# Performance work log

Measured on AMD Instinct MI355X. Metric: run time of the kernel, lower is better.

## Reference

```python
import jax, jax.numpy as jnp
import numpy as np

B, P, D = 256, 256, 514          # batch, num_patches (16^2), model_dim
H, HD = 8, 64                    # n_heads, head_dim ((D-2)//H)
SH = 256                         # shared_hidden = head_mlp_hidden_dims[0]
HH = 256                         # per-head hidden (head_mlp_hidden_dims[1])
DFF = 2048                       # ffn hidden
LH = 2 * SH                      # lat_modulator hidden = shared_hidden*2
LD = D - 2                       # learnable_dim

def gelu(x):
    return jax.nn.gelu(x, approximate=False)  # torch nn.GELU default is exact erf

def setup_inputs() -> dict:
    key = jax.random.key(0)
    ks = jax.random.split(key, 16)
    s = 0.02
    x = jax.random.normal(ks[0], (B, P, D), dtype=jnp.float32)
    # shared spatial layer: Linear(P -> SH), torch weight layout [out, in]
    Ws = jax.random.normal(ks[1], (SH, P), dtype=jnp.float32) * s
    bs = jax.random.normal(ks[2], (SH,), dtype=jnp.float32) * s
    # lat modulator: Linear(2 -> LH), GELU, Linear(LH -> 2*SH) with special init
    LW1 = jax.random.normal(ks[3], (LH, 2), dtype=jnp.float32) * s
    Lb1 = jax.random.normal(ks[4], (LH,), dtype=jnp.float32) * s
    LW2 = jnp.zeros((2 * SH, LH), dtype=jnp.float32)  # zeroed per module init
    Lb2 = jnp.concatenate([jnp.ones((SH,), jnp.float32), jnp.zeros((SH,), jnp.float32)])
    # per-head processing: Linear(SH->HH), GELU, Linear(HH->P), stacked over heads
    HW1 = jax.random.normal(ks[5], (H, HH, SH), dtype=jnp.float32) * s
    Hb1 = jax.random.normal(ks[6], (H, HH), dtype=jnp.float32) * s
    HW2 = jax.random.normal(ks[7], (H, P, HH), dtype=jnp.float32) * s
    Hb2 = jax.random.normal(ks[8], (H, P), dtype=jnp.float32) * s
    # ffn: Linear(D -> DFF) with last-2 input cols zeroed, GELU, Linear(DFF -> LD)
    FW1 = jax.random.normal(ks[9], (DFF, D), dtype=jnp.float32) * s
    FW1 = FW1.at[:, -2:].set(0.0)
    Fb1 = jax.random.normal(ks[10], (DFF,), dtype=jnp.float32) * s
    FW2 = jax.random.normal(ks[11], (LD, DFF), dtype=jnp.float32) * s
    Fb2 = jax.random.normal(ks[12], (LD,), dtype=jnp.float32) * s
    return dict(x=x, Ws=Ws, bs=bs, LW1=LW1, Lb1=Lb1, LW2=LW2, Lb2=Lb2,
                HW1=HW1, Hb1=Hb1, HW2=HW2, Hb2=Hb2,
                FW1=FW1, Fb1=Fb1, FW2=FW2, Fb2=Fb2)

def reference(x, Ws, bs, LW1, Lb1, LW2, Lb2, HW1, Hb1, HW2, Hb2, FW1, Fb1, FW2, Fb2):
    central = P // 2
    sc_central = x[:, central, -2:]          # [B, 2]
    sc_all = x[:, :, -2:]                    # [B, P, 2]
    x_learn = x[:, :, :-2]                   # [B, P, LD]
    x_res = x_learn
    # all heads at once: [B, P, H, HD] -> [B, H, HD, P]
    xh = x_learn.reshape(B, P, H, HD).transpose(0, 2, 3, 1)
    shared = jnp.einsum('bhdp,op->bhdo', xh, Ws) + bs   # [B, H, HD, SH]
    # FiLM params (loop-invariant in original, hoisted here)
    mod = gelu(sc_central @ LW1.T + Lb1) @ LW2.T + Lb2  # [B, 2*SH]
    gamma = mod[:, :SH][:, None, None, :]
    beta = mod[:, SH:][:, None, None, :]
    shared = shared * gamma + beta
    # per-head MLPs as grouped GEMMs
    h = gelu(jnp.einsum('bhdo,hko->bhdk', shared, HW1) + Hb1[None, :, None, :])
    out = jnp.einsum('bhdk,hpk->bhdp', h, HW2) + Hb2[None, :, None, :]  # [B,H,HD,P]
    x_learn = out.transpose(0, 3, 1, 2).reshape(B, P, LD) + x_res
    x_full = jnp.concatenate([x_learn, sc_all], axis=-1)  # [B, P, D]
    f = gelu(x_full @ FW1.T + Fb1) @ FW2.T + Fb2          # [B, P, LD]
    x_learn = f + x_learn
    return jnp.concatenate([x_learn, sc_all], axis=-1)
```

## Files before the change

kernel.cpp:

```cpp
#include <hip/hip_runtime.h>
#include <math.h>

typedef __attribute__((ext_vector_type(8))) __bf16 bf16x8;
typedef __attribute__((ext_vector_type(4))) float f32x4;
typedef __attribute__((ext_vector_type(2))) float f32x2;

#define DEV __device__ __forceinline__

typedef __attribute__((address_space(3))) unsigned int lds_u32;
typedef __attribute__((address_space(1))) unsigned int glb_u32;

DEV unsigned short f2bf(float f) {
    unsigned int u = __builtin_bit_cast(unsigned int, f);
    u += 0x7FFFu + ((u >> 16) & 1u);
    return (unsigned short)(u >> 16);
}
DEV float bf2f(unsigned short u) {
    unsigned int v = (unsigned int)u << 16;
    return __builtin_bit_cast(float, v);
}
DEV unsigned int pack2(float a, float b) {
    return (unsigned int)f2bf(a) | ((unsigned int)f2bf(b) << 16);
}
DEV float gelu_exact(float v) {
    return 0.5f * v * (1.0f + erff(v * 0.70710678118654752f));
}
DEV float gelu_fast(float x) {
    float z = 1.5957691216f * x + 0.0713548163f * x * x * x;
    float e = __expf(-z);
    return x * __builtin_amdgcn_rcpf(1.0f + e);
}

__global__ void cast_bf16_kernel(const float* __restrict__ src,
                                 unsigned short* __restrict__ dst, int n) {
    int i = blockIdx.x * 256 + threadIdx.x;
    if (i < n) dst[i] = f2bf(src[i]);
}

__global__ void cast_fw1_kernel(const float* __restrict__ src,
                                unsigned short* __restrict__ dst) {
    int i = blockIdx.x * 256 + threadIdx.x;
    if (i < 2048 * 512) {
        int row = i >> 9, k = i & 511;
        dst[i] = f2bf(src[row * 514 + k]);
    }
}

__global__ void gb_kernel(const float* __restrict__ x,
                          const float* __restrict__ LW1, const float* __restrict__ Lb1,
                          const float* __restrict__ LW2, const float* __restrict__ Lb2,
                          float* __restrict__ gb) {
    __shared__ float t[8][512];
    const int b0 = blockIdx.x * 8, tid = threadIdx.x;
    for (int idx = tid; idx < 8 * 512; idx += 256) {
        int bb = idx >> 9, j = idx & 511;
        float s0 = x[((size_t)(b0 + bb) * 256 + 128) * 514 + 512];
        float s1 = x[((size_t)(b0 + bb) * 256 + 128) * 514 + 513];
        t[bb][j] = gelu_exact(LW1[j * 2] * s0 + LW1[j * 2 + 1] * s1 + Lb1[j]);
    }
    __syncthreads();
    const int i = tid;
    float a0[8], a1[8];
    float l0 = Lb2[i], l1 = Lb2[i + 256];
    #pragma unroll
    for (int bb = 0; bb < 8; ++bb) { a0[bb] = l0; a1[bb] = l1; }
    for (int j = 0; j < 512; ++j) {
        float w0 = LW2[(size_t)i * 512 + j];
        float w1 = LW2[(size_t)(i + 256) * 512 + j];
        #pragma unroll
        for (int bb = 0; bb < 8; ++bb) {
            a0[bb] += w0 * t[bb][j];
            a1[bb] += w1 * t[bb][j];
        }
    }
    #pragma unroll
    for (int bb = 0; bb < 8; ++bb) {
        gb[(size_t)(b0 + bb) * 512 + i] = a0[bb];
        gb[(size_t)(b0 + bb) * 512 + i + 256] = a1[bb];
    }
}

__global__ void sc_copy_kernel(const float* __restrict__ x, float* __restrict__ out,
                               float* __restrict__ scbuf) {
    size_t idx = (size_t)blockIdx.x * 256 + threadIdx.x;
    size_t off = idx * 514 + 512;
    f32x2 v = *(const f32x2*)(x + off);
    *(f32x2*)(out + off) = v;
    *(f32x2*)(scbuf + idx * 2) = v;
}

#define MPAD 264

__global__ __launch_bounds__(256, 2) void mixer_kernel(
    const float* __restrict__ x, const float* __restrict__ bs,
    const float* __restrict__ Hb1, const float* __restrict__ Hb2,
    const unsigned short* __restrict__ Wsb,
    const unsigned short* __restrict__ HW1b,
    const unsigned short* __restrict__ HW2b,
    const float* __restrict__ gb,
    unsigned short* __restrict__ Xb) {
    __shared__ __attribute__((aligned(16))) char smem[33792 + 34816];
    unsigned short* XT = (unsigned short*)smem;
    unsigned short* S = (unsigned short*)(smem + 33792);
    unsigned short* ST = S;

    const int bid = blockIdx.x;
    const int b = bid >> 3;
    const int h = bid & 7;
    const int tid = threadIdx.x;
    const int lane = tid & 63;
    const int w = tid >> 6;
    const int l15 = lane & 15;
    const int l4 = lane >> 4;

    {
        const int c = lane;
        const float* xp = x + ((size_t)b * 256) * 514 + (size_t)h * 64 + c;
        for (int i = 0; i < 32; ++i) {
            int p = (i * 4 + w) * 2;
            float v0 = xp[(size_t)p * 514];
            float v1 = xp[(size_t)(p + 1) * 514];
            *(unsigned int*)&XT[c * MPAD + p] = pack2(v0, v1);
        }
    }
    __syncthreads();

    f32x4 acc[4][4];

    #pragma unroll
    for (int mt = 0; mt < 4; ++mt)
        #pragma unroll
        for (int nt = 0; nt < 4; ++nt) acc[mt][nt] = 0.f;
    {
        bf16x8 bnx[4];
        #pragma unroll
        for (int nt = 0; nt < 4; ++nt)
            bnx[nt] = *(const bf16x8*)(Wsb + (size_t)(w * 64 + nt * 16 + l15) * 256 + l4 * 8);
        for (int kc = 0; kc < 8; ++kc) {
            bf16x8 bcur[4];
            #pragma unroll
            for (int nt = 0; nt < 4; ++nt) bcur[nt] = bnx[nt];
            if (kc < 7) {
                #pragma unroll
                for (int nt = 0; nt < 4; ++nt)
                    bnx[nt] = *(const bf16x8*)(Wsb + (size_t)(w * 64 + nt * 16 + l15) * 256 + (kc + 1) * 32 + l4 * 8);
            }
            #pragma unroll
            for (int mt = 0; mt < 4; ++mt) {
                bf16x8 afr = *(const bf16x8*)&XT[(mt * 16 + l15) * MPAD + kc * 32 + l4 * 8];
                #pragma unroll
                for (int nt = 0; nt < 4; ++nt)
                    acc[mt][nt] = __builtin_amdgcn_mfma_f32_16x16x32_bf16(afr, bcur[nt], acc[mt][nt], 0, 0, 0);
            }
        }
    }
    #pragma unroll
    for (int nt = 0; nt < 4; ++nt) {
        int o = w * 64 + nt * 16 + l15;
        float bsv = bs[o];
        float g = gb[(size_t)b * 512 + o];
        float be = gb[(size_t)b * 512 + 256 + o];
        #pragma unroll
        for (int mt = 0; mt < 4; ++mt)
            #pragma unroll
            for (int r = 0; r < 4; ++r) {
                int c = mt * 16 + l4 * 4 + r;
                S[c * MPAD + o] = f2bf((acc[mt][nt][r] + bsv) * g + be);
            }
    }
    __syncthreads();

    const unsigned short* W2p = HW1b + (size_t)h * 65536;
    #pragma unroll
    for (int mt = 0; mt < 4; ++mt)
        #pragma unroll
        for (int nt = 0; nt < 4; ++nt) acc[mt][nt] = 0.f;
    {
        bf16x8 bnx[4];
        #pragma unroll
        for (int nt = 0; nt < 4; ++nt)
            bnx[nt] = *(const bf16x8*)(W2p + (size_t)(w * 64 + nt * 16 + l15) * 256 + l4 * 8);
        for (int kc = 0; kc < 8; ++kc) {
            bf16x8 bcur[4];
            #pragma unroll
            for (int nt = 0; nt < 4; ++nt) bcur[nt] = bnx[nt];
            if (kc < 7) {
                #pragma unroll
                for (int nt = 0; nt < 4; ++nt)
                    bnx[nt] = *(const bf16x8*)(W2p + (size_t)(w * 64 + nt * 16 + l15) * 256 + (kc + 1) * 32 + l4 * 8);
            }
            #pragma unroll
            for (int mt = 0; mt < 4; ++mt) {
                bf16x8 afr = *(const bf16x8*)&S[(mt * 16 + l15) * MPAD + kc * 32 + l4 * 8];
                #pragma unroll
                for (int nt = 0; nt < 4; ++nt)
                    acc[mt][nt] = __builtin_amdgcn_mfma_f32_16x16x32_bf16(afr, bcur[nt], acc[mt][nt], 0, 0, 0);
            }
        }
    }
    __syncthreads();
    #pragma unroll
    for (int nt = 0; nt < 4; ++nt) {
        int kk = w * 64 + nt * 16 + l15;
        float hb = Hb1[(size_t)h * 256 + kk];
        #pragma unroll
        for (int mt = 0; mt < 4; ++mt)
            #pragma unroll
            for (int r = 0; r < 4; ++r) {
                int c = mt * 16 + l4 * 4 + r;
                S[c * MPAD + kk] = f2bf(gelu_fast(acc[mt][nt][r] + hb));
            }
    }
    __syncthreads();

    const unsigned short* W3p = HW2b + (size_t)h * 65536;
    #pragma unroll
    for (int mt = 0; mt < 4; ++mt)
        #pragma unroll
        for (int nt = 0; nt < 4; ++nt) acc[mt][nt] = 0.f;
    {
        bf16x8 bnx[4];
        #pragma unroll
        for (int nt = 0; nt < 4; ++nt)
            bnx[nt] = *(const bf16x8*)(W3p + (size_t)(w * 64 + nt * 16 + l15) * 256 + l4 * 8);
        for (int kc = 0; kc < 8; ++kc) {
            bf16x8 bcur[4];
            #pragma unroll
            for (int nt = 0; nt < 4; ++nt) bcur[nt] = bnx[nt];
            if (kc < 7) {
                #pragma unroll
                for (int nt = 0; nt < 4; ++nt)
                    bnx[nt] = *(const bf16x8*)(W3p + (size_t)(w * 64 + nt * 16 + l15) * 256 + (kc + 1) * 32 + l4 * 8);
            }
            #pragma unroll
            for (int mt = 0; mt < 4; ++mt) {
                bf16x8 afr = *(const bf16x8*)&S[(mt * 16 + l15) * MPAD + kc * 32 + l4 * 8];
                #pragma unroll
                for (int nt = 0; nt < 4; ++nt)
                    acc[mt][nt] = __builtin_amdgcn_mfma_f32_16x16x32_bf16(afr, bcur[nt], acc[mt][nt], 0, 0, 0);
            }
        }
    }
    __syncthreads();

    #pragma unroll
    for (int nt = 0; nt < 4; ++nt) {
        int p = w * 64 + nt * 16 + l15;
        float hb = Hb2[(size_t)h * 256 + p];
        #pragma unroll
        for (int mt = 0; mt < 4; ++mt) {
            int c0 = mt * 16 + l4 * 4;
            ushort4 uv;
            uv.x = f2bf(acc[mt][nt][0] + hb + bf2f(XT[(c0 + 0) * MPAD + p]));
            uv.y = f2bf(acc[mt][nt][1] + hb + bf2f(XT[(c0 + 1) * MPAD + p]));
            uv.z = f2bf(acc[mt][nt][2] + hb + bf2f(XT[(c0 + 2) * MPAD + p]));
            uv.w = f2bf(acc[mt][nt][3] + hb + bf2f(XT[(c0 + 3) * MPAD + p]));
            *(ushort4*)(ST + p * 68 + c0) = uv;
        }
    }
    __syncthreads();

    #pragma unroll
    for (int s = 0; s < 16; ++s) {
        int row = s * 16 + w * 4 + l4;
        ushort4 u = *(const ushort4*)(ST + row * 68 + l15 * 4);
        *(ushort4*)(Xb + ((size_t)(b * 256 + row)) * 512 + h * 64 + l15 * 4) = u;
    }
}

DEV void stage_half(const unsigned short* g, size_t gstride, int row0, int k0,
                    char* half_base, int w, int lane) {
    const int slot = lane & 7;
    const int r8 = lane >> 3;
    const int swz = (slot ^ r8) * 16;
    #pragma unroll
    for (int i = 0; i < 2; ++i) {
        int chunk = w * 2 + i;
        int row = chunk * 8 + r8;
        const char* src = (const char*)(g + (size_t)(row0 + row) * gstride + k0) + swz;
        __builtin_amdgcn_global_load_lds((const glb_u32*)src,
                                         (lds_u32*)(half_base + chunk * 1024), 16, 0, 0);
    }
}

DEV void stage4(const unsigned short* A, size_t sA, int m0,
                const unsigned short* B, size_t sB, int n0, int k0,
                char* Abuf, char* Bbuf, int w, int lane) {
    stage_half(A, sA, m0, k0, Abuf, w, lane);
    stage_half(A, sA, m0 + 128, k0, Abuf + 16384, w, lane);
    stage_half(B, sB, n0, k0, Bbuf, w, lane);
    stage_half(B, sB, n0 + 128, k0, Bbuf + 16384, w, lane);
}

DEV void tile_body(const unsigned short* A, size_t sA, int m0,
                   const unsigned short* B, size_t sB, int n0,
                   char* smem, int cb, int kn, bool more,
                   int vA0, int vA1, int vB0, int vB1,
                   int w, int lane, f32x4 (&acc)[8][4]) {
    if (more) {
        int nb = 32768 - cb;
        stage4(A, sA, m0, B, sB, n0, kn, smem + nb, smem + 65536 + nb, w, lane);
    }
    __builtin_amdgcn_s_setprio(1);
    #pragma unroll
    for (int kk = 0; kk < 2; ++kk) {
        const int vA = kk ? vA1 : vA0;
        const int vB = kk ? vB1 : vB0;
        bf16x8 bf[4];
        #pragma unroll
        for (int nf = 0; nf < 4; ++nf)
            bf[nf] = *(const bf16x8*)(smem + vB + cb + nf * 2048);
        #pragma unroll
        for (int mh = 0; mh < 2; ++mh) {
            bf16x8 af[4];
            #pragma unroll
            for (int mf = 0; mf < 4; ++mf)
                af[mf] = *(const bf16x8*)(smem + vA + cb + mh * 8192 + mf * 2048);
            #pragma unroll
            for (int mf = 0; mf < 4; ++mf)
                #pragma unroll
                for (int nf = 0; nf < 4; ++nf)
                    acc[mh * 4 + mf][nf] = __builtin_amdgcn_mfma_f32_16x16x32_bf16(
                        af[mf], bf[nf], acc[mh * 4 + mf][nf], 0, 0, 0);
        }
    }
    __builtin_amdgcn_s_setprio(0);
    if (more) asm volatile("s_waitcnt vmcnt(0)" ::: "memory");
    __builtin_amdgcn_s_barrier();
}

DEV void gemm_loop(const unsigned short* A, size_t sA,
                   const unsigned short* B, size_t sB,
                   int m0, int n0, int NT,
                   char* smem, int w, int lane, f32x4 (&acc)[8][4]) {
    const int wm = w >> 2, wn = w & 3;
    const int l15 = lane & 15, l4 = lane >> 4;
    const int sw = (l15 & 7) << 4;
    const int k0off = (l4 * 16) ^ sw;
    const int k1off = (64 + l4 * 16) ^ sw;
    const int aBase = (wm * 128 + l15) * 128;
    const int bBase = 65536 + (wn * 64 + l15) * 128;
    const int vA0 = aBase + k0off, vA1 = aBase + k1off;
    const int vB0 = bBase + k0off, vB1 = bBase + k1off;

    stage4(A, sA, m0, B, sB, n0, 0, smem, smem + 65536, w, lane);
    asm volatile("s_waitcnt vmcnt(0)" ::: "memory");
    __builtin_amdgcn_s_barrier();

    for (int t = 0; t < NT; t += 2) {
        tile_body(A, sA, m0, B, sB, n0, smem, 0, (t + 1) * 64, t + 1 < NT,
                  vA0, vA1, vB0, vB1, w, lane, acc);
        tile_body(A, sA, m0, B, sB, n0, smem, 32768, (t + 2) * 64, t + 2 < NT,
                  vA0, vA1, vB0, vB1, w, lane, acc);
    }
}

__global__ __launch_bounds__(512, 1) void gemm1_kernel(
    const unsigned short* __restrict__ A,
    const unsigned short* __restrict__ B,
    const float* __restrict__ Fb1,
    const float* __restrict__ FW1,
    const float* __restrict__ scbuf,
    long pass_m0,
    unsigned short* __restrict__ G) {
    __shared__ __attribute__((aligned(16))) char smem[131072];

    const int nwg = gridDim.x;
    const int cpx = nwg >> 3;
    const int bid = (blockIdx.x & 7) * cpx + (blockIdx.x >> 3);
    const int m0 = (bid >> 3) * 256;
    const int n0 = (bid & 7) * 256;
    const int tid = threadIdx.x;
    const int lane = tid & 63;
    const int w = tid >> 6;
    const int l15 = lane & 15;
    const int l4 = lane >> 4;
    const int wm = w >> 2, wn = w & 3;

    f32x4 acc[8][4];
    #pragma unroll
    for (int mf = 0; mf < 8; ++mf)
        #pragma unroll
        for (int nf = 0; nf < 4; ++nf) acc[mf][nf] = 0.f;

    gemm_loop(A, 512, B, 512, m0, n0, 8, smem, w, lane, acc);

    float fb[4], wa[4], wb[4];
    #pragma unroll
    for (int nf = 0; nf < 4; ++nf) {
        int n = n0 + wn * 64 + nf * 16 + l15;
        fb[nf] = Fb1[n];
        wa[nf] = FW1[(size_t)n * 514 + 512];
        wb[nf] = FW1[(size_t)n * 514 + 513];
    }
    unsigned short* LT = (unsigned short*)smem;
    #pragma unroll
    for (int ph = 0; ph < 2; ++ph) {
        if (wm == ph) {
            #pragma unroll
            for (int mfg = 0; mfg < 8; ++mfg) {
                f32x2 sc[4];
                #pragma unroll
                for (int r = 0; r < 4; ++r) {
                    long rowg = pass_m0 + m0 + ph * 128 + mfg * 16 + l4 * 4 + r;
                    sc[r] = *(const f32x2*)(scbuf + rowg * 2);
                }
                #pragma unroll
                for (int nf = 0; nf < 4; ++nf)
                    #pragma unroll
                    for (int r = 0; r < 4; ++r) {
                        float v = acc[mfg][nf][r] + fb[nf] + sc[r].x * wa[nf] + sc[r].y * wb[nf];
                        int rl = mfg * 16 + l4 * 4 + r;
                        LT[rl * 264 + wn * 64 + nf * 16 + l15] = f2bf(gelu_fast(v));
                    }
            }
        }
        __syncthreads();
        {
            const int row16 = tid >> 5, col16 = tid & 31;
            #pragma unroll
            for (int sp = 0; sp < 8; ++sp) {
                int row = sp * 16 + row16;
                uint4 d = *(const uint4*)((const char*)smem + row * 528 + col16 * 16);
                *(uint4*)(G + ((size_t)(m0 + ph * 128 + row)) * 2048 + n0 + col16 * 8) = d;
            }
        }
        __syncthreads();
    }
}

__global__ __launch_bounds__(512, 1) void gemm2_kernel(
    const unsigned short* __restrict__ A,
    const unsigned short* __restrict__ B,
    const float* __restrict__ Fb2,
    const unsigned short* __restrict__ Xb,
    long pass_m0,
    float* __restrict__ io) {
    __shared__ __attribute__((aligned(16))) char smem[131072];

    const int nwg = gridDim.x;
    const int cpx = nwg >> 3;
    const int bid = (blockIdx.x & 7) * cpx + (blockIdx.x >> 3);
    const int m0 = (bid >> 1) * 256;
    const int n0 = (bid & 1) * 256;
    const int tid = threadIdx.x;
    const int lane = tid & 63;
    const int w = tid >> 6;
    const int l15 = lane & 15;
    const int l4 = lane >> 4;
    const int wm = w >> 2, wn = w & 3;

    f32x4 acc[8][4];
    #pragma unroll
    for (int mf = 0; mf < 8; ++mf)
        #pragma unroll
        for (int nf = 0; nf < 4; ++nf) acc[mf][nf] = 0.f;

    gemm_loop(A, 2048, B, 2048, m0, n0, 32, smem, w, lane, acc);

    #pragma unroll
    for (int nf = 0; nf < 4; ++nf) {
        int n = n0 + wn * 64 + nf * 16 + l15;
        float fbv = Fb2[n];
        #pragma unroll
        for (int mfg = 0; mfg < 8; ++mfg)
            #pragma unroll
            for (int r = 0; r < 4; ++r) {
                long rowg = pass_m0 + m0 + wm * 128 + mfg * 16 + l4 * 4 + r;
                float resv = bf2f(Xb[(size_t)rowg * 512 + n]);
                io[rowg * 514 + n] = acc[mfg][nf][r] + fbv + resv;
            }
    }
}

extern "C" void kernel_launch(void* const* d_in, const int* in_sizes, int n_in,
                              void* d_out, int out_size, void* d_ws, size_t ws_size,
                              hipStream_t stream) {
    const float* x = (const float*)d_in[0];
    const float* Ws = (const float*)d_in[1];
    const float* bs = (const float*)d_in[2];
    const float* LW1 = (const float*)d_in[3];
    const float* Lb1 = (const float*)d_in[4];
    const float* LW2 = (const float*)d_in[5];
    const float* Lb2 = (const float*)d_in[6];
    const float* HW1 = (const float*)d_in[7];
    const float* Hb1 = (const float*)d_in[8];
    const float* HW2 = (const float*)d_in[9];
    const float* Hb2 = (const float*)d_in[10];
    const float* FW1 = (const float*)d_in[11];
    const float* Fb1 = (const float*)d_in[12];
    const float* FW2 = (const float*)d_in[13];
    const float* Fb2 = (const float*)d_in[14];
    float* out = (float*)d_out;

    char* ws = (char*)d_ws;
    unsigned short* Wsb = (unsigned short*)(ws);
    unsigned short* HW1b = (unsigned short*)(ws + 131072);
    unsigned short* HW2b = (unsigned short*)(ws + 1179648);
    unsigned short* FW1b = (unsigned short*)(ws + 2228224);
    unsigned short* FW2b = (unsigned short*)(ws + 4325376);
    float* gb = (float*)(ws + 6422528);
    float* scbuf = (float*)(ws + 6946816);
    unsigned short* Xb = (unsigned short*)(ws + 7471104);
    unsigned short* Gbuf = (unsigned short*)(ws + 7471104 + 67108864);

    const size_t fixed = 7471104 + 67108864;
    int npass = 32;
    for (int np = 2; np <= 32; np *= 2) {
        if (fixed + (size_t)268435456 / np <= ws_size) { npass = np; break; }
    }
    const long Mtot = 65536;
    const long Mp = Mtot / npass;

    cast_bf16_kernel<<<256, 256, 0, stream>>>(Ws, Wsb, 65536);
    cast_bf16_kernel<<<2048, 256, 0, stream>>>(HW1, HW1b, 524288);
    cast_bf16_kernel<<<2048, 256, 0, stream>>>(HW2, HW2b, 524288);
    cast_bf16_kernel<<<4096, 256, 0, stream>>>(FW2, FW2b, 1048576);
    cast_fw1_kernel<<<4096, 256, 0, stream>>>(FW1, FW1b);
    gb_kernel<<<32, 256, 0, stream>>>(x, LW1, Lb1, LW2, Lb2, gb);
    sc_copy_kernel<<<256, 256, 0, stream>>>(x, out, scbuf);

    mixer_kernel<<<2048, 256, 0, stream>>>(x, bs, Hb1, Hb2, Wsb, HW1b, HW2b, gb, Xb);

    for (int p = 0; p < npass; ++p) {
        long m0 = (long)p * Mp;
        gemm1_kernel<<<(int)(Mp / 256) * 8, 512, 0, stream>>>(
            Xb + m0 * 512, FW1b, Fb1, FW1, scbuf, m0, Gbuf);
        gemm2_kernel<<<(int)(Mp / 256) * 2, 512, 0, stream>>>(
            Gbuf, FW2b, Fb2, Xb, m0, out);
    }
}
```

Baseline: 665.8 us.

## Shrink GEMM tiles to 128x128 with 256 threads and several blocks per CU

The FFN GEMM kernels drop the 256x256, 512-thread, single-block-per-CU double-buffered pipeline and use 128x128 tiles with 4 waves and a simple single-buffer stage/sync loop. Each block uses about 33KB of LDS, so three blocks can share a CU and overlap load latency through occupancy instead of explicit prefetch. The epilogues shrink to match, and the mixer's transposing load now reads 8 consecutive patches per thread and writes them with one 16-byte LDS store. In exchange the smaller tiles lower operand reuse, adding global and LDS traffic per FLOP, and the explicit software pipelining is lost.

```diff
diff --git a/kernel.cpp b/kernel.cpp
--- a/kernel.cpp
+++ b/kernel.cpp
@@ -116,11 +116,23 @@
     {
         const int c = lane;
         const float* xp = x + ((size_t)b * 256) * 514 + (size_t)h * 64 + c;
-        for (int i = 0; i < 32; ++i) {
-            int p = (i * 4 + w) * 2;
-            float v0 = xp[(size_t)p * 514];
-            float v1 = xp[(size_t)(p + 1) * 514];
-            *(unsigned int*)&XT[c * MPAD + p] = pack2(v0, v1);
+        #pragma unroll
+        for (int g = 0; g < 8; ++g) {
+            int p0 = w * 64 + g * 8;
+            float v0 = xp[(size_t)(p0 + 0) * 514];
+            float v1 = xp[(size_t)(p0 + 1) * 514];
+            float v2 = xp[(size_t)(p0 + 2) * 514];
+            float v3 = xp[(size_t)(p0 + 3) * 514];
+            float v4 = xp[(size_t)(p0 + 4) * 514];
+            float v5 = xp[(size_t)(p0 + 5) * 514];
+            float v6 = xp[(size_t)(p0 + 6) * 514];
+            float v7 = xp[(size_t)(p0 + 7) * 514];
+            uint4 pk;
+            pk.x = pack2(v0, v1);
+            pk.y = pack2(v2, v3);
+            pk.z = pack2(v4, v5);
+            pk.w = pack2(v6, v7);
+            *(uint4*)&XT[c * MPAD + p0] = pk;
         }
     }
     __syncthreads();
@@ -268,94 +280,60 @@
     }
 }
 
-DEV void stage_half(const unsigned short* g, size_t gstride, int row0, int k0,
-                    char* half_base, int w, int lane) {
-    const int slot = lane & 7;
-    const int r8 = lane >> 3;
+DEV void stage_m97(const unsigned short* g, size_t gstride, int row0, int k0,
+                   char* lbuf, int tid) {
+    const int slot = tid & 7;
+    const int r8 = (tid >> 3) & 7;
+    const int wv = tid >> 6;
     const int swz = (slot ^ r8) * 16;
     #pragma unroll
-    for (int i = 0; i < 2; ++i) {
-        int chunk = w * 2 + i;
+    for (int i = 0; i < 4; ++i) {
+        int chunk = i * 4 + wv;
         int row = chunk * 8 + r8;
         const char* src = (const char*)(g + (size_t)(row0 + row) * gstride + k0) + swz;
         __builtin_amdgcn_global_load_lds((const glb_u32*)src,
-                                         (lds_u32*)(half_base + chunk * 1024), 16, 0, 0);
-    }
-}
-
-DEV void stage4(const unsigned short* A, size_t sA, int m0,
-                const unsigned short* B, size_t sB, int n0, int k0,
-                char* Abuf, char* Bbuf, int w, int lane) {
-    stage_half(A, sA, m0, k0, Abuf, w, lane);
-    stage_half(A, sA, m0 + 128, k0, Abuf + 16384, w, lane);
-    stage_half(B, sB, n0, k0, Bbuf, w, lane);
-    stage_half(B, sB, n0 + 128, k0, Bbuf + 16384, w, lane);
-}
-
-DEV void tile_body(const unsigned short* A, size_t sA, int m0,
-                   const unsigned short* B, size_t sB, int n0,
-                   char* smem, int cb, int kn, bool more,
-                   int vA0, int vA1, int vB0, int vB1,
-                   int w, int lane, f32x4 (&acc)[8][4]) {
-    if (more) {
-        int nb = 32768 - cb;
-        stage4(A, sA, m0, B, sB, n0, kn, smem + nb, smem + 65536 + nb, w, lane);
-    }
-    __builtin_amdgcn_s_setprio(1);
-    #pragma unroll
-    for (int kk = 0; kk < 2; ++kk) {
-        const int vA = kk ? vA1 : vA0;
-        const int vB = kk ? vB1 : vB0;
-        bf16x8 bf[4];
-        #pragma unroll
-        for (int nf = 0; nf < 4; ++nf)
-            bf[nf] = *(const bf16x8*)(smem + vB + cb + nf * 2048);
-        #pragma unroll
-        for (int mh = 0; mh < 2; ++mh) {
-            bf16x8 af[4];
+                                         (lds_u32*)(lbuf + chunk * 1024), 16, 0, 0);
+    }
+}
+
+DEV void gemm_loop97(const unsigned short* A, size_t sA,
+                     const unsigned short* B, size_t sB,
+                     int m0, int n0, int NT,
+                     char* smem, int tid, f32x4 (&acc)[4][4]) {
+    const int lane = tid & 63;
+    const int w = tid >> 6;
+    const int l15 = lane & 15, l4 = lane >> 4;
+    const int wm = w >> 1, wn = w & 1;
+
+    for (int t = 0; t < NT; ++t) {
+        stage_m97(A, sA, m0, t * 64, smem, tid);
+        stage_m97(B, sB, n0, t * 64, smem + 16384, tid);
+        __syncthreads();
+        #pragma unroll
+        for (int kk = 0; kk < 2; ++kk) {
+            bf16x8 af[4], bf[4];
+            #pragma unroll
+            for (int mf = 0; mf < 4; ++mf) {
+                int row = wm * 64 + mf * 16 + l15;
+                af[mf] = *(const bf16x8*)(smem + row * 128 + ((kk * 64 + l4 * 16) ^ ((row & 7) << 4)));
+            }
+            #pragma unroll
+            for (int nf = 0; nf < 4; ++nf) {
+                int row = wn * 64 + nf * 16 + l15;
+                bf[nf] = *(const bf16x8*)(smem + 16384 + row * 128 + ((kk * 64 + l4 * 16) ^ ((row & 7) << 4)));
+            }
             #pragma unroll
             for (int mf = 0; mf < 4; ++mf)
-                af[mf] = *(const bf16x8*)(smem + vA + cb + mh * 8192 + mf * 2048);
-            #pragma unroll
-            for (int mf = 0; mf < 4; ++mf)
                 #pragma unroll
                 for (int nf = 0; nf < 4; ++nf)
-                    acc[mh * 4 + mf][nf] = __builtin_amdgcn_mfma_f32_16x16x32_bf16(
-                        af[mf], bf[nf], acc[mh * 4 + mf][nf], 0, 0, 0);
-        }
-    }
-    __builtin_amdgcn_s_setprio(0);
-    if (more) asm volatile("s_waitcnt vmcnt(0)" ::: "memory");
-    __builtin_amdgcn_s_barrier();
-}
-
-DEV void gemm_loop(const unsigned short* A, size_t sA,
-                   const unsigned short* B, size_t sB,
-                   int m0, int n0, int NT,
-                   char* smem, int w, int lane, f32x4 (&acc)[8][4]) {
-    const int wm = w >> 2, wn = w & 3;
-    const int l15 = lane & 15, l4 = lane >> 4;
-    const int sw = (l15 & 7) << 4;
-    const int k0off = (l4 * 16) ^ sw;
-    const int k1off = (64 + l4 * 16) ^ sw;
-    const int aBase = (wm * 128 + l15) * 128;
-    const int bBase = 65536 + (wn * 64 + l15) * 128;
-    const int vA0 = aBase + k0off, vA1 = aBase + k1off;
-    const int vB0 = bBase + k0off, vB1 = bBase + k1off;
-
-    stage4(A, sA, m0, B, sB, n0, 0, smem, smem + 65536, w, lane);
-    asm volatile("s_waitcnt vmcnt(0)" ::: "memory");
-    __builtin_amdgcn_s_barrier();
-
-    for (int t = 0; t < NT; t += 2) {
-        tile_body(A, sA, m0, B, sB, n0, smem, 0, (t + 1) * 64, t + 1 < NT,
-                  vA0, vA1, vB0, vB1, w, lane, acc);
-        tile_body(A, sA, m0, B, sB, n0, smem, 32768, (t + 2) * 64, t + 2 < NT,
-                  vA0, vA1, vB0, vB1, w, lane, acc);
-    }
-}
-
-__global__ __launch_bounds__(512, 1) void gemm1_kernel(
+                    acc[mf][nf] = __builtin_amdgcn_mfma_f32_16x16x32_bf16(
+                        af[mf], bf[nf], acc[mf][nf], 0, 0, 0);
+        }
+        __syncthreads();
+    }
+}
+
+__global__ __launch_bounds__(256, 3) void gemm1_kernel(
     const unsigned short* __restrict__ A,
     const unsigned short* __restrict__ B,
     const float* __restrict__ Fb1,
@@ -363,27 +341,27 @@
     const float* __restrict__ scbuf,
     long pass_m0,
     unsigned short* __restrict__ G) {
-    __shared__ __attribute__((aligned(16))) char smem[131072];
+    __shared__ __attribute__((aligned(16))) char smem[34816];
 
     const int nwg = gridDim.x;
     const int cpx = nwg >> 3;
     const int bid = (blockIdx.x & 7) * cpx + (blockIdx.x >> 3);
-    const int m0 = (bid >> 3) * 256;
-    const int n0 = (bid & 7) * 256;
+    const int m0 = (bid >> 4) * 128;
+    const int n0 = (bid & 15) * 128;
     const int tid = threadIdx.x;
     const int lane = tid & 63;
     const int w = tid >> 6;
     const int l15 = lane & 15;
     const int l4 = lane >> 4;
-    const int wm = w >> 2, wn = w & 3;
-
-    f32x4 acc[8][4];
-    #pragma unroll
-    for (int mf = 0; mf < 8; ++mf)
+    const int wm = w >> 1, wn = w & 1;
+
+    f32x4 acc[4][4];
+    #pragma unroll
+    for (int mf = 0; mf < 4; ++mf)
         #pragma unroll
         for (int nf = 0; nf < 4; ++nf) acc[mf][nf] = 0.f;
 
-    gemm_loop(A, 512, B, 512, m0, n0, 8, smem, w, lane, acc);
+    gemm_loop97(A, 512, B, 512, m0, n0, 8, smem, tid, acc);
 
     float fb[4], wa[4], wb[4];
     #pragma unroll
@@ -393,82 +371,77 @@
         wa[nf] = FW1[(size_t)n * 514 + 512];
         wb[nf] = FW1[(size_t)n * 514 + 513];
     }
+    f32x2 sc[4][4];
+    #pragma unroll
+    for (int mf = 0; mf < 4; ++mf)
+        #pragma unroll
+        for (int r = 0; r < 4; ++r) {
+            long rowg = pass_m0 + m0 + wm * 64 + mf * 16 + l4 * 4 + r;
+            sc[mf][r] = *(const f32x2*)(scbuf + rowg * 2);
+        }
     unsigned short* LT = (unsigned short*)smem;
     #pragma unroll
-    for (int ph = 0; ph < 2; ++ph) {
-        if (wm == ph) {
-            #pragma unroll
-            for (int mfg = 0; mfg < 8; ++mfg) {
-                f32x2 sc[4];
-                #pragma unroll
-                for (int r = 0; r < 4; ++r) {
-                    long rowg = pass_m0 + m0 + ph * 128 + mfg * 16 + l4 * 4 + r;
-                    sc[r] = *(const f32x2*)(scbuf + rowg * 2);
-                }
-                #pragma unroll
-                for (int nf = 0; nf < 4; ++nf)
-                    #pragma unroll
-                    for (int r = 0; r < 4; ++r) {
-                        float v = acc[mfg][nf][r] + fb[nf] + sc[r].x * wa[nf] + sc[r].y * wb[nf];
-                        int rl = mfg * 16 + l4 * 4 + r;
-                        LT[rl * 264 + wn * 64 + nf * 16 + l15] = f2bf(gelu_fast(v));
-                    }
-            }
-        }
-        __syncthreads();
-        {
-            const int row16 = tid >> 5, col16 = tid & 31;
-            #pragma unroll
-            for (int sp = 0; sp < 8; ++sp) {
-                int row = sp * 16 + row16;
-                uint4 d = *(const uint4*)((const char*)smem + row * 528 + col16 * 16);
-                *(uint4*)(G + ((size_t)(m0 + ph * 128 + row)) * 2048 + n0 + col16 * 8) = d;
-            }
-        }
-        __syncthreads();
-    }
-}
-
-__global__ __launch_bounds__(512, 1) void gemm2_kernel(
+    for (int mf = 0; mf < 4; ++mf)
+        #pragma unroll
+        for (int nf = 0; nf < 4; ++nf)
+            #pragma unroll
+            for (int r = 0; r < 4; ++r) {
+                float v = acc[mf][nf][r] + fb[nf] + sc[mf][r].x * wa[nf] + sc[mf][r].y * wb[nf];
+                int rl = wm * 64 + mf * 16 + l4 * 4 + r;
+                LT[rl * 136 + wn * 64 + nf * 16 + l15] = f2bf(gelu_fast(v));
+            }
+    __syncthreads();
+    {
+        const int lane16 = tid & 15, rowq = tid >> 4;
+        #pragma unroll
+        for (int s = 0; s < 8; ++s) {
+            int row = s * 16 + rowq;
+            uint4 d = *(const uint4*)((const char*)smem + row * 272 + lane16 * 16);
+            *(uint4*)(G + ((size_t)(m0 + row)) * 2048 + n0 + lane16 * 8) = d;
+        }
+    }
+}
+
+__global__ __launch_bounds__(256, 3) void gemm2_kernel(
     const unsigned short* __restrict__ A,
     const unsigned short* __restrict__ B,
     const float* __restrict__ Fb2,
     const unsigned short* __restrict__ Xb,
     long pass_m0,
     float* __restrict__ io) {
-    __shared__ __attribute__((aligned(16))) char smem[131072];
+    __shared__ __attribute__((aligned(16))) char smem[32768];
 
     const int nwg = gridDim.x;
     const int cpx = nwg >> 3;
     const int bid = (blockIdx.x & 7) * cpx + (blockIdx.x >> 3);
-    const int m0 = (bid >> 1) * 256;
-    const int n0 = (bid & 1) * 256;
+    const int m0 = (bid >> 2) * 128;
+    const int n0 = (bid & 3) * 128;
     const int tid = threadIdx.x;
     const int lane = tid & 63;
     const int w = tid >> 6;
     const int l15 = lane & 15;
     const int l4 = lane >> 4;
-    const int wm = w >> 2, wn = w & 3;
-
-    f32x4 acc[8][4];
-    #pragma unroll
-    for (int mf = 0; mf < 8; ++mf)
+    const int wm = w >> 1, wn = w & 1;
+
+    f32x4 acc[4][4];
+    #pragma unroll
+    for (int mf = 0; mf < 4; ++mf)
         #pragma unroll
         for (int nf = 0; nf < 4; ++nf) acc[mf][nf] = 0.f;
 
-    gemm_loop(A, 2048, B, 2048, m0, n0, 32, smem, w, lane, acc);
+    gemm_loop97(A, 2048, B, 2048, m0, n0, 32, smem, tid, acc);
 
     #pragma unroll
     for (int nf = 0; nf < 4; ++nf) {
         int n = n0 + wn * 64 + nf * 16 + l15;
         float fbv = Fb2[n];
         #pragma unroll
-        for (int mfg = 0; mfg < 8; ++mfg)
+        for (int mf = 0; mf < 4; ++mf)
             #pragma unroll
             for (int r = 0; r < 4; ++r) {
-                long rowg = pass_m0 + m0 + wm * 128 + mfg * 16 + l4 * 4 + r;
+                long rowg = pass_m0 + m0 + wm * 64 + mf * 16 + l4 * 4 + r;
                 float resv = bf2f(Xb[(size_t)rowg * 512 + n]);
-                io[rowg * 514 + n] = acc[mfg][nf][r] + fbv + resv;
+                io[rowg * 514 + n] = acc[mf][nf][r] + fbv + resv;
             }
     }
 }
@@ -524,9 +497,9 @@
 
     for (int p = 0; p < npass; ++p) {
         long m0 = (long)p * Mp;
-        gemm1_kernel<<<(int)(Mp / 256) * 8, 512, 0, stream>>>(
+        gemm1_kernel<<<(int)(Mp / 128) * 16, 256, 0, stream>>>(
             Xb + m0 * 512, FW1b, Fb1, FW1, scbuf, m0, Gbuf);
-        gemm2_kernel<<<(int)(Mp / 256) * 2, 512, 0, stream>>>(
+        gemm2_kernel<<<(int)(Mp / 128) * 4, 256, 0, stream>>>(
             Gbuf, FW2b, Fb2, Xb, m0, out);
     }
 }
```

New measurement: 601.1 us. 1.11x faster.
